# Kernel tuning notes

Hardware: AMD Instinct MI355X
Metric: run time of the kernel (lower is better)

Reference implementation:

```python
import jax, jax.numpy as jnp
import numpy as np

B, T, D, H = 2, 2048, 1024, 16


def setup_inputs() -> dict:
    key = jax.random.key(0)
    ks = jax.random.split(key, 5)
    s = 0.02  # small init so softmax is well-behaved
    return {
        "x": jax.random.normal(ks[0], (B, T, D), dtype=jnp.float32),
        "Wq": jax.random.normal(ks[1], (D, D), dtype=jnp.float32) * s,
        "bq": jnp.zeros((D,), dtype=jnp.float32),
        "Wk": jax.random.normal(ks[2], (D, D), dtype=jnp.float32) * s,
        "bk": jnp.zeros((D,), dtype=jnp.float32),
        "Wv": jax.random.normal(ks[3], (D, D), dtype=jnp.float32) * s,
        "bv": jnp.zeros((D,), dtype=jnp.float32),
        "Wo": jax.random.normal(ks[4], (D, D), dtype=jnp.float32) * s,
        "bo": jnp.zeros((D,), dtype=jnp.float32),
    }


def _split_heads(t):
    # (B,T,D) -> (B,H,T,d_k)
    b, tt, dd = t.shape
    return t.reshape(b, tt, H, dd // H).transpose(0, 2, 1, 3)


def reference(x, Wq, bq, Wk, bk, Wv, bv, Wo, bo):
    d_k = D // H
    q = _split_heads(x @ Wq + bq)  # (B,H,T,d_k)
    k = _split_heads(x @ Wk + bk)
    v = _split_heads(x @ Wv + bv)
    # scaled dot-product similarities: (B,H,T,T)
    scores = jnp.einsum("bhqd,bhkd->bhqk", q, k) / jnp.sqrt(jnp.asarray(d_k, dtype=x.dtype))
    causal = jnp.tril(jnp.ones((T, T), dtype=bool))  # True = keep
    scores = jnp.where(causal, scores, jnp.asarray(-jnp.inf, dtype=scores.dtype))
    probs = jax.nn.softmax(scores, axis=-1)
    attn = jnp.einsum("bhqk,bhkd->bhqd", probs, v)  # (B,H,T,d_k)
    merged = attn.transpose(0, 2, 1, 3).reshape(B, T, D)  # (B,T,D)
    return merged @ Wo + bo
```

## Files before the change

kernel.cpp:

```cpp
#include <hip/hip_runtime.h>
#include <hip/hip_bf16.h>
#include <cstdint>
#include <cstddef>

#define B_  2
#define T_  2048
#define D_  1024
#define H_  16
#define DK_ 64

typedef __hip_bfloat16 bf16;
typedef __bf16 bf16x8 __attribute__((ext_vector_type(8)));
typedef float  f32x4  __attribute__((ext_vector_type(4)));

#define MFMA16(a, b, c) __builtin_amdgcn_mfma_f32_16x16x32_bf16((a), (b), (c), 0, 0, 0)

#define SCALE_Q 0.1803368801111137f

#if defined(__has_builtin)
#if __has_builtin(__builtin_amdgcn_exp2f)
#define FEXP2(x) __builtin_amdgcn_exp2f(x)
#endif
#endif
#ifndef FEXP2
__device__ static inline float fexp2_asm(float x) {
  float r; asm("v_exp_f32 %0, %1" : "=v"(r) : "v"(x)); return r;
}
#define FEXP2(x) fexp2_asm(x)
#endif

__device__ static inline void gld_lds16(const void* g, void* l) {
  __builtin_amdgcn_global_load_lds((const __attribute__((address_space(1))) void*)g,
                                   (__attribute__((address_space(3))) void*)l, 16, 0, 0);
}

__device__ static inline ushort f2bu(float x) {
  union { bf16 h; ushort u; } c;
  c.h = __float2bfloat16(x);
  return c.u;
}

__device__ static inline uint32_t cvtpk_bf16(float lo, float hi) {
  uint32_t r;
  asm volatile("v_cvt_pk_bf16_f32 %0, %1, %2" : "=v"(r) : "v"(lo), "v"(hi));
  return r;
}

__global__ __launch_bounds__(256) void pack_x_kernel(const float* __restrict__ x,
                                                     bf16* __restrict__ xb) {
  const int i = blockIdx.x * 256 + threadIdx.x;
  const float4 v = reinterpret_cast<const float4*>(x)[i];
  union { ushort4 u; bf16 h[4]; } c;
  c.h[0] = __float2bfloat16(v.x);
  c.h[1] = __float2bfloat16(v.y);
  c.h[2] = __float2bfloat16(v.z);
  c.h[3] = __float2bfloat16(v.w);
  reinterpret_cast<ushort4*>(xb)[i] = c.u;
}

__global__ __launch_bounds__(256) void pack_w_kernel(const float* __restrict__ Wq,
                                                     const float* __restrict__ Wk,
                                                     const float* __restrict__ Wv,
                                                     const float* __restrict__ Wo,
                                                     bf16* __restrict__ Wt,
                                                     bf16* __restrict__ Wot) {
  __shared__ bf16 t[64][65];
  const int bid  = blockIdx.x;
  const int mat  = bid >> 8;
  const int tile = bid & 255;
  const int tr = tile >> 4, tc = tile & 15;
  const float* W = (mat == 0) ? Wq : (mat == 1) ? Wk : (mat == 2) ? Wv : Wo;
  const int tid = threadIdx.x;
#pragma unroll
  for (int i = 0; i < 16; ++i) {
    const int idx = i * 256 + tid;
    const int r = idx >> 6, c = idx & 63;
    t[r][c] = __float2bfloat16(W[(size_t)(tr * 64 + r) * D_ + tc * 64 + c]);
  }
  __syncthreads();
  bf16* dst = (mat == 3) ? Wot : (Wt + (size_t)mat * D_ * D_);
#pragma unroll
  for (int i = 0; i < 16; ++i) {
    const int idx = i * 256 + tid;
    const int n = idx >> 6, k = idx & 63;
    dst[(size_t)(tc * 64 + n) * D_ + tr * 64 + k] = t[k][n];
  }
}

__global__ __launch_bounds__(256, 3) void gemm_qkv_kernel(
    const bf16* __restrict__ A, const bf16* __restrict__ Bt,
    const float* __restrict__ bias0, const float* __restrict__ bias1,
    const float* __restrict__ bias2,
    bf16* __restrict__ Qb, bf16* __restrict__ Kb, bf16* __restrict__ Vt) {
  __shared__ bf16 As[128 * 32];
  __shared__ bf16 Bs[128 * 32];
  const int tid  = threadIdx.x;
  const int lane = tid & 63, wid = tid >> 6;
  const int wr = wid >> 1, wc = wid & 1;
  const int l15 = lane & 15, lhi = lane >> 4;
  const int mbase = blockIdx.y * 128, nbase = blockIdx.x * 128;

  f32x4 acc[4][4] = {};

  const int r0  = tid >> 2;
  const int kc0 = (tid & 3) * 8;
  char* AsB = (char*)As;
  char* BsB = (char*)Bs;

  for (int kt = 0; kt < D_; kt += 32) {
    gld_lds16(A  + (size_t)(mbase + r0)      * D_ + kt + kc0, AsB + wid * 1024);
    gld_lds16(A  + (size_t)(mbase + 64 + r0) * D_ + kt + kc0, AsB + 4096 + wid * 1024);
    gld_lds16(Bt + (size_t)(nbase + r0)      * D_ + kt + kc0, BsB + wid * 1024);
    gld_lds16(Bt + (size_t)(nbase + 64 + r0) * D_ + kt + kc0, BsB + 4096 + wid * 1024);
    __syncthreads();

    bf16x8 af[4], bfv[4];
#pragma unroll
    for (int m = 0; m < 4; ++m)
      af[m] = *reinterpret_cast<const bf16x8*>(&As[(wr * 64 + m * 16 + l15) * 32 + lhi * 8]);
#pragma unroll
    for (int n = 0; n < 4; ++n)
      bfv[n] = *reinterpret_cast<const bf16x8*>(&Bs[(wc * 64 + n * 16 + l15) * 32 + lhi * 8]);
#pragma unroll
    for (int m = 0; m < 4; ++m)
#pragma unroll
      for (int n = 0; n < 4; ++n)
        acc[m][n] = MFMA16(af[m], bfv[n], acc[m][n]);
    __syncthreads();
  }

#pragma unroll
  for (int n = 0; n < 4; ++n) {
    const int col = nbase + wc * 64 + n * 16 + l15;
    const int seg  = col >> 10;
    const int ncol = col & 1023;
    const float* bias = (seg == 0) ? bias0 : (seg == 1) ? bias1 : bias2;
    const float bv_ = bias[ncol];
    const int h = ncol >> 6, dk = ncol & 63;
    if (seg == 2) {
#pragma unroll
      for (int m = 0; m < 4; ++m) {
        const int t0 = mbase + wr * 64 + m * 16 + lhi * 4;
        const int b = t0 >> 11, t = t0 & 2047;
        union { ushort u[4]; uint2 v; } pk;
#pragma unroll
        for (int j = 0; j < 4; ++j) pk.u[j] = f2bu(acc[m][n][j] + bv_);
        *reinterpret_cast<uint2*>(&Vt[((size_t)(b * H_ + h) * DK_ + dk) * T_ + t]) = pk.v;
      }
    } else {
#pragma unroll
      for (int m = 0; m < 4; ++m) {
#pragma unroll
        for (int j = 0; j < 4; ++j) {
          const int row = mbase + wr * 64 + m * 16 + lhi * 4 + j;
          const int b = row >> 11, t = row & 2047;
          const int bh = b * H_ + h;
          float outv = acc[m][n][j] + bv_;
          if (seg == 0) outv *= SCALE_Q;
          const bf16 hv = __float2bfloat16(outv);
          if (seg == 0) Qb[((size_t)bh * T_ + t) * DK_ + dk] = hv;
          else          Kb[((size_t)bh * T_ + t) * DK_ + dk] = hv;
        }
      }
    }
  }
}

__global__ __launch_bounds__(256, 2) void gemm_out_kernel(
    const bf16* __restrict__ A, const bf16* __restrict__ Bt,
    const float* __restrict__ bias, float* __restrict__ outp) {
  __shared__ bf16 As[128 * 32];
  __shared__ bf16 Bs[64 * 32];
  const int tid  = threadIdx.x;
  const int lane = tid & 63, wid = tid >> 6;
  const int wr = wid >> 1, wc = wid & 1;
  const int l15 = lane & 15, lhi = lane >> 4;
  const int mbase = blockIdx.y * 128, nbase = blockIdx.x * 64;

  f32x4 acc[4][2] = {};

  const int r0  = tid >> 2;
  const int kc0 = (tid & 3) * 8;
  char* AsB = (char*)As;
  char* BsB = (char*)Bs;

  for (int kt = 0; kt < D_; kt += 32) {
    gld_lds16(A  + (size_t)(mbase + r0)      * D_ + kt + kc0, AsB + wid * 1024);
    gld_lds16(A  + (size_t)(mbase + 64 + r0) * D_ + kt + kc0, AsB + 4096 + wid * 1024);
    gld_lds16(Bt + (size_t)(nbase + r0)      * D_ + kt + kc0, BsB + wid * 1024);
    __syncthreads();

    bf16x8 af[4], bfv[2];
#pragma unroll
    for (int m = 0; m < 4; ++m)
      af[m] = *reinterpret_cast<const bf16x8*>(&As[(wr * 64 + m * 16 + l15) * 32 + lhi * 8]);
#pragma unroll
    for (int n = 0; n < 2; ++n)
      bfv[n] = *reinterpret_cast<const bf16x8*>(&Bs[(wc * 32 + n * 16 + l15) * 32 + lhi * 8]);
#pragma unroll
    for (int m = 0; m < 4; ++m)
#pragma unroll
      for (int n = 0; n < 2; ++n)
        acc[m][n] = MFMA16(af[m], bfv[n], acc[m][n]);
    __syncthreads();
  }

#pragma unroll
  for (int n = 0; n < 2; ++n) {
    const int col = nbase + wc * 32 + n * 16 + l15;
    const float bv_ = bias[col];
#pragma unroll
    for (int m = 0; m < 4; ++m)
#pragma unroll
      for (int j = 0; j < 4; ++j) {
        const int row = mbase + wr * 64 + m * 16 + lhi * 4 + j;
        outp[(size_t)row * D_ + col] = acc[m][n][j] + bv_;
      }
  }
}

__global__ __launch_bounds__(512, 4) void attn_kernel(const bf16* __restrict__ Q,
                                                      const bf16* __restrict__ Kg,
                                                      const bf16* __restrict__ Vt,
                                                      bf16* __restrict__ Mg) {
  __shared__ __align__(16) bf16 Kl[2][128 * 64];
  __shared__ __align__(16) bf16 Vl[2][64 * 128];
  const int tid = threadIdx.x, lane = tid & 63, wid = tid >> 6;
  const int l15 = lane & 15, lhi = lane >> 4;
  const int p  = blockIdx.x & 15;
  const int bh = blockIdx.x >> 4;
  const int half = wid >> 2, w4 = wid & 3;
  const int qtile = half ? (31 - p) : p;
  const int qbase = qtile * 64 + w4 * 16;
  const int b = bh >> 4, h = bh & 15;

  const bf16* Qp = Q  + (size_t)bh * T_ * DK_;
  const bf16* Kp = Kg + (size_t)bh * T_ * DK_;
  const bf16* Vp = Vt + (size_t)bh * DK_ * T_;

  const bf16x8 qf0 = *reinterpret_cast<const bf16x8*>(&Qp[(size_t)(qbase + l15) * DK_ + lhi * 8]);
  const bf16x8 qf1 = *reinterpret_cast<const bf16x8*>(&Qp[(size_t)(qbase + l15) * DK_ + 32 + lhi * 8]);

  bf16x8 onesb;
#pragma unroll
  for (int i = 0; i < 8; ++i) onesb[i] = (__bf16)1.0f;

  f32x4 o[4] = {};
  f32x4 lacc = {};
  float mrow = -1e30f;

  const int ntr = (33 - p) >> 1;

  const int iA = tid, iB = 512 + tid;
  const bf16* ks0 = Kp + (size_t)(iA >> 3) * DK_ + (((iA & 7) ^ ((iA >> 3) & 7)) * 8);
  const bf16* ks1 = Kp + (size_t)(iB >> 3) * DK_ + (((iB & 7) ^ ((iB >> 3) & 7)) * 8);
  const bf16* vs0 = Vp + (size_t)(iA >> 4) * T_ + (((iA & 15) ^ ((iA >> 4) & 15)) * 8);
  const bf16* vs1 = Vp + (size_t)(iB >> 4) * T_ + (((iB & 15) ^ ((iB >> 4) & 15)) * 8);
  const int ub0 = wid * 1024;
  const int ub1 = 8192 + wid * 1024;

  gld_lds16(ks0, (char*)Kl[0] + ub0);
  gld_lds16(ks1, (char*)Kl[0] + ub1);
  gld_lds16(vs0, (char*)Vl[0] + ub0);
  gld_lds16(vs1, (char*)Vl[0] + ub1);
  ks0 += 128 * DK_; ks1 += 128 * DK_; vs0 += 128; vs1 += 128;
  __syncthreads();

  for (int rnd = 0; rnd < ntr; ++rnd) {
    const int cur = rnd & 1;
    const char* Kb_ = cur ? (const char*)Kl[1] : (const char*)Kl[0];
    const char* Vb_ = cur ? (const char*)Vl[1] : (const char*)Vl[0];
    if (rnd + 1 < ntr) {
      char* Kn = cur ? (char*)Kl[0] : (char*)Kl[1];
      char* Vn = cur ? (char*)Vl[0] : (char*)Vl[1];
      gld_lds16(ks0, Kn + ub0);
      gld_lds16(ks1, Kn + ub1);
      gld_lds16(vs0, Vn + ub0);
      gld_lds16(vs1, Vn + ub1);
      ks0 += 128 * DK_; ks1 += 128 * DK_; vs0 += 128; vs1 += 128;
    }

#pragma unroll
    for (int sub = 0; sub < 2; ++sub) {
      const int kv0 = rnd * 128 + sub * 64;
      if (kv0 <= qbase + 15) {
        f32x4 sv[4];
#pragma unroll
        for (int s = 0; s < 4; ++s) {
          const int cbase = kv0 + s * 16;
          if (cbase <= qbase + 15) {
            const int row = sub * 64 + s * 16 + l15;
            const int rsw = l15 & 7;
            const bf16x8 k0 = *reinterpret_cast<const bf16x8*>(Kb_ + row * 128 + ((lhi       ^ rsw) * 16));
            const bf16x8 k1 = *reinterpret_cast<const bf16x8*>(Kb_ + row * 128 + (((4 + lhi) ^ rsw) * 16));
            f32x4 z = {};
            z = MFMA16(k0, qf0, z);
            sv[s] = MFMA16(k1, qf1, z);
          } else {
#pragma unroll
            for (int j = 0; j < 4; ++j) sv[s][j] = -1e30f;
          }
        }

#pragma unroll
        for (int s = 0; s < 4; ++s) {
          const int cbase = kv0 + s * 16;
          if (cbase <= qbase + 15 && cbase + 15 > qbase) {
            const int r = qbase + l15;
#pragma unroll
            for (int j = 0; j < 4; ++j) {
              const int c = cbase + lhi * 4 + j;
              sv[s][j] = (c <= r) ? sv[s][j] : -1e30f;
            }
          }
        }

        float ml = sv[0][0];
#pragma unroll
        for (int s = 0; s < 4; ++s)
#pragma unroll
          for (int j = 0; j < 4; ++j) ml = fmaxf(ml, sv[s][j]);

        if (__any(ml > mrow + 8.0f)) {
          float mx = ml;
          mx = fmaxf(mx, __shfl_xor(mx, 16, 64));
          mx = fmaxf(mx, __shfl_xor(mx, 32, 64));
          const float mn = fmaxf(mrow, mx);
          const float sc = FEXP2(mrow - mn);
          mrow = mn;
          const int sci = __float_as_int(sc);
#pragma unroll
          for (int j = 0; j < 4; ++j) {
            const float scj = __int_as_float(
                __builtin_amdgcn_ds_bpermute((lhi * 4 + j) * 4, sci));
            lacc[j] *= scj;
            o[0][j] *= scj; o[1][j] *= scj; o[2][j] *= scj; o[3][j] *= scj;
          }
        }
#pragma unroll
        for (int s = 0; s < 4; ++s)
#pragma unroll
          for (int j = 0; j < 4; ++j) sv[s][j] = FEXP2(sv[s][j] - mrow);

        const bool oddl = (lhi & 1) != 0;
        bf16x8 pf[2];
#pragma unroll
        for (int hh = 0; hh < 2; ++hh) {
          const uint32_t u0l = cvtpk_bf16(sv[2 * hh][0], sv[2 * hh][1]);
          const uint32_t u0h = cvtpk_bf16(sv[2 * hh][2], sv[2 * hh][3]);
          const uint32_t u1l = cvtpk_bf16(sv[2 * hh + 1][0], sv[2 * hh + 1][1]);
          const uint32_t u1h = cvtpk_bf16(sv[2 * hh + 1][2], sv[2 * hh + 1][3]);
          const uint32_t sl = oddl ? u0l : u1l;
          const uint32_t sh = oddl ? u0h : u1h;
          const uint32_t rl = (uint32_t)__shfl_xor((int)sl, 16, 64);
          const uint32_t rh = (uint32_t)__shfl_xor((int)sh, 16, 64);
          union { uint32_t w[4]; bf16x8 v; } fr;
          fr.w[0] = oddl ? rl : u0l;
          fr.w[1] = oddl ? rh : u0h;
          fr.w[2] = oddl ? u1l : rl;
          fr.w[3] = oddl ? u1h : rh;
          pf[hh] = fr.v;
        }

        const int pl = ((lhi & 1) << 1) | (lhi >> 1);
        bf16x8 vf[8];
#pragma unroll
        for (int d = 0; d < 4; ++d) {
          const int rowv = d * 16 + l15;
#pragma unroll
          for (int s2 = 0; s2 < 2; ++s2) {
            const int cread = sub * 8 + s2 * 4 + pl;
            vf[d * 2 + s2] = *reinterpret_cast<const bf16x8*>(
                Vb_ + rowv * 256 + ((cread ^ l15) * 16));
          }
        }

#pragma unroll
        for (int d = 0; d < 4; ++d) {
          o[d] = MFMA16(pf[0], vf[d * 2 + 0], o[d]);
          o[d] = MFMA16(pf[1], vf[d * 2 + 1], o[d]);
        }
        lacc = MFMA16(pf[0], onesb, lacc);
        lacc = MFMA16(pf[1], onesb, lacc);
      }
    }

    __syncthreads();
  }

#pragma unroll
  for (int j = 0; j < 4; ++j) {
    const float inv = 1.0f / lacc[j];
    const int tq = qbase + lhi * 4 + j;
#pragma unroll
    for (int d = 0; d < 4; ++d)
      Mg[((size_t)b * T_ + tq) * D_ + h * DK_ + d * 16 + l15] = __float2bfloat16(o[d][j] * inv);
  }
}

extern "C" void kernel_launch(void* const* d_in, const int* in_sizes, int n_in,
                              void* d_out, int out_size, void* d_ws, size_t ws_size,
                              hipStream_t stream) {
  (void)in_sizes; (void)n_in; (void)out_size; (void)ws_size;
  const float* x  = (const float*)d_in[0];
  const float* Wq = (const float*)d_in[1];
  const float* bq = (const float*)d_in[2];
  const float* Wk = (const float*)d_in[3];
  const float* bk = (const float*)d_in[4];
  const float* Wv = (const float*)d_in[5];
  const float* bv = (const float*)d_in[6];
  const float* Wo = (const float*)d_in[7];
  const float* bo = (const float*)d_in[8];
  float* out = (float*)d_out;

  char* ws = (char*)d_ws;
  bf16* xb  = (bf16*)(ws);
  bf16* Mg  = (bf16*)(ws);
  bf16* Wt  = (bf16*)(ws + (size_t)( 8u << 20));
  bf16* Wot = (bf16*)(ws + (size_t)(14u << 20));
  bf16* Qb  = (bf16*)(ws + (size_t)(16u << 20));
  bf16* Kb  = (bf16*)(ws + (size_t)(24u << 20));
  bf16* Vt  = (bf16*)(ws + (size_t)(32u << 20));

  pack_x_kernel<<<4096, 256, 0, stream>>>(x, xb);
  pack_w_kernel<<<1024, 256, 0, stream>>>(Wq, Wk, Wv, Wo, Wt, Wot);
  gemm_qkv_kernel<<<dim3(24, 32), 256, 0, stream>>>(xb, Wt, bq, bk, bv, Qb, Kb, Vt);
  attn_kernel<<<dim3(512), 512, 0, stream>>>(Qb, Kb, Vt, Mg);
  gemm_out_kernel<<<dim3(16, 32), 256, 0, stream>>>(Mg, Wot, bo, out);
}
```

Measured before the change: 112.9 us.

## Rewrite QKV GEMM with 256x256 tiles, double-buffered LDS, and swizzled layout

The QKV projection GEMM moves from 128x128 tiles with a single LDS buffer and BK=32 to 256x256 tiles with 8 waves, BK=64, and double-buffered LDS. Each k-step is split into four phases that interleave the next tile's global-to-LDS loads with MFMA work, and it uses XOR-swizzled LDS addressing, s_setprio, and a block-index swizzle for L2 locality. The aim is to hide memory latency, cut LDS bank conflicts and raise data reuse per block. The cost is 128KB of LDS and far fewer blocks (192), which could underfill the GPU.

```diff
diff --git a/kernel.cpp b/kernel.cpp
--- a/kernel.cpp
+++ b/kernel.cpp
@@ -87,75 +87,115 @@
   }
 }
 
-__global__ __launch_bounds__(256, 3) void gemm_qkv_kernel(
+__global__ __launch_bounds__(512, 2) void gemm_qkv_kernel(
     const bf16* __restrict__ A, const bf16* __restrict__ Bt,
     const float* __restrict__ bias0, const float* __restrict__ bias1,
     const float* __restrict__ bias2,
     bf16* __restrict__ Qb, bf16* __restrict__ Kb, bf16* __restrict__ Vt) {
-  __shared__ bf16 As[128 * 32];
-  __shared__ bf16 Bs[128 * 32];
-  const int tid  = threadIdx.x;
-  const int lane = tid & 63, wid = tid >> 6;
-  const int wr = wid >> 1, wc = wid & 1;
+  __shared__ __align__(16) bf16 Asm[2][2][128 * 64];
+  __shared__ __align__(16) bf16 Bsm[2][2][128 * 64];
+  const int tid = threadIdx.x, lane = tid & 63, wid = tid >> 6;
   const int l15 = lane & 15, lhi = lane >> 4;
-  const int mbase = blockIdx.y * 128, nbase = blockIdx.x * 128;
-
-  f32x4 acc[4][4] = {};
-
-  const int r0  = tid >> 2;
-  const int kc0 = (tid & 3) * 8;
-  char* AsB = (char*)As;
-  char* BsB = (char*)Bs;
-
-  for (int kt = 0; kt < D_; kt += 32) {
-    gld_lds16(A  + (size_t)(mbase + r0)      * D_ + kt + kc0, AsB + wid * 1024);
-    gld_lds16(A  + (size_t)(mbase + 64 + r0) * D_ + kt + kc0, AsB + 4096 + wid * 1024);
-    gld_lds16(Bt + (size_t)(nbase + r0)      * D_ + kt + kc0, BsB + wid * 1024);
-    gld_lds16(Bt + (size_t)(nbase + 64 + r0) * D_ + kt + kc0, BsB + 4096 + wid * 1024);
-    __syncthreads();
-
-    bf16x8 af[4], bfv[4];
-#pragma unroll
-    for (int m = 0; m < 4; ++m)
-      af[m] = *reinterpret_cast<const bf16x8*>(&As[(wr * 64 + m * 16 + l15) * 32 + lhi * 8]);
-#pragma unroll
-    for (int n = 0; n < 4; ++n)
-      bfv[n] = *reinterpret_cast<const bf16x8*>(&Bs[(wc * 64 + n * 16 + l15) * 32 + lhi * 8]);
-#pragma unroll
-    for (int m = 0; m < 4; ++m)
-#pragma unroll
-      for (int n = 0; n < 4; ++n)
-        acc[m][n] = MFMA16(af[m], bfv[n], acc[m][n]);
-    __syncthreads();
-  }
-
-#pragma unroll
-  for (int n = 0; n < 4; ++n) {
-    const int col = nbase + wc * 64 + n * 16 + l15;
-    const int seg  = col >> 10;
+  const int wm = wid >> 2, wn = wid & 3;
+
+  const int flat = blockIdx.x + blockIdx.y * 12;
+  const int swz = (flat & 7) * 24 + (flat >> 3);
+  const int mbase = (swz / 12) * 256;
+  const int nbase = (swz % 12) * 256;
+
+  const int i0 = tid, i1 = 512 + tid;
+  const int r0 = i0 >> 3, cs0 = ((i0 & 7) ^ (r0 & 7)) * 8;
+  const int r1 = i1 >> 3, cs1 = ((i1 & 7) ^ (r1 & 7)) * 8;
+  const bf16* spA00 = A  + (size_t)(mbase +       r0) * D_ + cs0;
+  const bf16* spA01 = A  + (size_t)(mbase +       r1) * D_ + cs1;
+  const bf16* spA10 = A  + (size_t)(mbase + 128 + r0) * D_ + cs0;
+  const bf16* spA11 = A  + (size_t)(mbase + 128 + r1) * D_ + cs1;
+  const bf16* spB00 = Bt + (size_t)(nbase +       r0) * D_ + cs0;
+  const bf16* spB01 = Bt + (size_t)(nbase +       r1) * D_ + cs1;
+  const bf16* spB10 = Bt + (size_t)(nbase + 128 + r0) * D_ + cs0;
+  const bf16* spB11 = Bt + (size_t)(nbase + 128 + r1) * D_ + cs1;
+  const int ub0 = wid * 1024;
+  const int ub1 = 8192 + wid * 1024;
+
+  f32x4 acc[8][4] = {};
+
+  gld_lds16(spA00, (char*)Asm[0][0] + ub0); gld_lds16(spA01, (char*)Asm[0][0] + ub1);
+  gld_lds16(spA10, (char*)Asm[0][1] + ub0); gld_lds16(spA11, (char*)Asm[0][1] + ub1);
+  gld_lds16(spB00, (char*)Bsm[0][0] + ub0); gld_lds16(spB01, (char*)Bsm[0][0] + ub1);
+  gld_lds16(spB10, (char*)Bsm[0][1] + ub0); gld_lds16(spB11, (char*)Bsm[0][1] + ub1);
+  asm volatile("s_waitcnt vmcnt(0)" ::: "memory");
+  __builtin_amdgcn_s_barrier();
+
+#define PHASE(db, mh, nh, DO_ST, DST, SP0, SP1, KO, DO_VM)                               \
+  {                                                                                      \
+    const char* Ah = (const char*)Asm[db][wm];                                           \
+    const char* Bh = (const char*)Bsm[db][wn >> 1];                                      \
+    bf16x8 afr[4][2], bfr[2][2];                                                         \
+    _Pragma("unroll") for (int m4 = 0; m4 < 4; ++m4)                                     \
+      _Pragma("unroll") for (int kk = 0; kk < 2; ++kk)                                   \
+        afr[m4][kk] = *reinterpret_cast<const bf16x8*>(                                  \
+            Ah + ((mh) * 64 + m4 * 16 + l15) * 128 + (((kk * 4 + lhi) ^ (l15 & 7)) * 16)); \
+    _Pragma("unroll") for (int n2 = 0; n2 < 2; ++n2)                                     \
+      _Pragma("unroll") for (int kk = 0; kk < 2; ++kk)                                   \
+        bfr[n2][kk] = *reinterpret_cast<const bf16x8*>(                                  \
+            Bh + ((wn & 1) * 64 + ((nh) * 2 + n2) * 16 + l15) * 128 +                    \
+                 (((kk * 4 + lhi) ^ (l15 & 7)) * 16));                                   \
+    if (DO_ST) {                                                                         \
+      gld_lds16((SP0) + (KO), (char*)(DST) + ub0);                                       \
+      gld_lds16((SP1) + (KO), (char*)(DST) + ub1);                                       \
+    }                                                                                    \
+    __builtin_amdgcn_s_barrier();                                                        \
+    asm volatile("s_waitcnt lgkmcnt(0)" ::: "memory");                                   \
+    __builtin_amdgcn_sched_barrier(0);                                                   \
+    __builtin_amdgcn_s_setprio(1);                                                       \
+    _Pragma("unroll") for (int n2 = 0; n2 < 2; ++n2)                                     \
+      _Pragma("unroll") for (int m4 = 0; m4 < 4; ++m4)                                   \
+        _Pragma("unroll") for (int kk = 0; kk < 2; ++kk)                                 \
+          acc[(mh) * 4 + m4][(nh) * 2 + n2] =                                            \
+              MFMA16(afr[m4][kk], bfr[n2][kk], acc[(mh) * 4 + m4][(nh) * 2 + n2]);       \
+    __builtin_amdgcn_s_setprio(0);                                                       \
+    if (DO_VM) asm volatile("s_waitcnt vmcnt(0)" ::: "memory");                          \
+    __builtin_amdgcn_s_barrier();                                                        \
+  }
+
+  for (int t = 0; t < 16; ++t) {
+    const int db = t & 1, nb = db ^ 1;
+    const bool st = (t < 15);
+    const int ko = (t + 1) * 64;
+    PHASE(db, 0, 0, st, Asm[nb][0], spA00, spA01, ko, false);
+    PHASE(db, 1, 0, st, Asm[nb][1], spA10, spA11, ko, false);
+    PHASE(db, 0, 1, st, Bsm[nb][0], spB00, spB01, ko, false);
+    PHASE(db, 1, 1, st, Bsm[nb][1], spB10, spB11, ko, true);
+  }
+#undef PHASE
+
+  const int seg = nbase >> 10;
+  const float* bias = (seg == 0) ? bias0 : (seg == 1) ? bias1 : bias2;
+#pragma unroll
+  for (int nf = 0; nf < 4; ++nf) {
+    const int col  = nbase + wn * 64 + nf * 16 + l15;
     const int ncol = col & 1023;
-    const float* bias = (seg == 0) ? bias0 : (seg == 1) ? bias1 : bias2;
     const float bv_ = bias[ncol];
     const int h = ncol >> 6, dk = ncol & 63;
     if (seg == 2) {
 #pragma unroll
-      for (int m = 0; m < 4; ++m) {
-        const int t0 = mbase + wr * 64 + m * 16 + lhi * 4;
+      for (int mf = 0; mf < 8; ++mf) {
+        const int t0 = mbase + wm * 128 + mf * 16 + lhi * 4;
         const int b = t0 >> 11, t = t0 & 2047;
         union { ushort u[4]; uint2 v; } pk;
 #pragma unroll
-        for (int j = 0; j < 4; ++j) pk.u[j] = f2bu(acc[m][n][j] + bv_);
+        for (int j = 0; j < 4; ++j) pk.u[j] = f2bu(acc[mf][nf][j] + bv_);
         *reinterpret_cast<uint2*>(&Vt[((size_t)(b * H_ + h) * DK_ + dk) * T_ + t]) = pk.v;
       }
     } else {
 #pragma unroll
-      for (int m = 0; m < 4; ++m) {
+      for (int mf = 0; mf < 8; ++mf) {
 #pragma unroll
         for (int j = 0; j < 4; ++j) {
-          const int row = mbase + wr * 64 + m * 16 + lhi * 4 + j;
+          const int row = mbase + wm * 128 + mf * 16 + lhi * 4 + j;
           const int b = row >> 11, t = row & 2047;
           const int bh = b * H_ + h;
-          float outv = acc[m][n][j] + bv_;
+          float outv = acc[mf][nf][j] + bv_;
           if (seg == 0) outv *= SCALE_Q;
           const bf16 hv = __float2bfloat16(outv);
           if (seg == 0) Qb[((size_t)bh * T_ + t) * DK_ + dk] = hv;
@@ -424,7 +464,7 @@
 
   pack_x_kernel<<<4096, 256, 0, stream>>>(x, xb);
   pack_w_kernel<<<1024, 256, 0, stream>>>(Wq, Wk, Wv, Wo, Wt, Wot);
-  gemm_qkv_kernel<<<dim3(24, 32), 256, 0, stream>>>(xb, Wt, bq, bk, bv, Qb, Kb, Vt);
+  gemm_qkv_kernel<<<dim3(12, 16), 512, 0, stream>>>(xb, Wt, bq, bk, bv, Qb, Kb, Vt);
   attn_kernel<<<dim3(512), 512, 0, stream>>>(Qb, Kb, Vt, Mg);
   gemm_out_kernel<<<dim3(16, 32), 256, 0, stream>>>(Mg, Wot, bo, out);
 }
```

New measurement: 117.2 us. 3.7% more time.
